# Kernel tuning notes

Hardware: AMD Instinct MI355X
Metric: run time of the kernel (lower is better)

The kernel has to match this reference:

```python
import jax, jax.numpy as jnp
import numpy as np

B, NC, DC = 4, 1024, 256      # batch, codebook entries, codebook dim
K, L = 512, 128               # num_latents, latent_dim
NP, Q = 65536, 64             # query points, queries_dim
LH = 8                        # latent self-attn heads (dim_head 64)
LN_EPS = 1e-5


def _ln(x, g, b):
    m = jnp.mean(x, axis=-1, keepdims=True)
    v = jnp.var(x, axis=-1, keepdims=True)
    return (x - m) * jax.lax.rsqrt(v + LN_EPS) * g + b


def _attn(x, ctx, wq, wkv, wo, bo, h):
    # x: [b,n,dq], ctx: [b,j,dc]; wq: [dq, h*d], wkv: [dc, 2*h*d]
    b, n, _ = x.shape
    j = ctx.shape[1]
    d = wq.shape[1] // h
    q = (x @ wq).reshape(b, n, h, d)
    k, v = jnp.split(ctx @ wkv, 2, axis=-1)
    k = k.reshape(b, j, h, d)
    v = v.reshape(b, j, h, d)
    sim = jnp.einsum('bihd,bjhd->bhij', q, k) * (d ** -0.5)
    a = jax.nn.softmax(sim, axis=-1)
    o = jnp.einsum('bhij,bjhd->bihd', a, v).reshape(b, n, h * d)
    return o @ wo + bo


def _geglu(x):
    a, g = jnp.split(x, 2, axis=-1)
    return a * jax.nn.gelu(g, approximate=False)  # torch F.gelu is exact erf


def setup_inputs() -> dict:
    key = jax.random.key(0)
    ks = iter(jax.random.split(key, 32))
    def w(shape):  # kaiming-ish scaled randn, [in, out] layout
        return jax.random.normal(next(ks), shape, jnp.float32) / np.sqrt(shape[0]).astype(np.float32)
    inp = {
        'codebook': jax.random.normal(next(ks), (B, NC, DC), jnp.float32),
        'queries': jax.random.normal(next(ks), (B, NP, Q), jnp.float32),
        'latents': jax.random.normal(next(ks), (K, L), jnp.float32),
        # CodebookAttention: cross-attn (PreNorm with context norm)
        'ca_ng': jnp.ones((L,)), 'ca_nb': jnp.zeros((L,)),
        'ca_cng': jnp.ones((DC,)), 'ca_cnb': jnp.zeros((DC,)),
        'ca_wq': w((L, 64)), 'ca_wkv': w((DC, 128)), 'ca_wo': w((64, L)), 'ca_bo': jnp.zeros((L,)),
        # cross FF (GEGLU, mult=4)
        'cf_ng': jnp.ones((L,)), 'cf_nb': jnp.zeros((L,)),
        'cf_w1': w((L, 8 * L)), 'cf_b1': jnp.zeros((8 * L,)),
        'cf_w2': w((4 * L, L)), 'cf_b2': jnp.zeros((L,)),
        # latent self-attn (8 heads x 64)
        'sa_ng': jnp.ones((L,)), 'sa_nb': jnp.zeros((L,)),
        'sa_wq': w((L, 512)), 'sa_wkv': w((L, 1024)), 'sa_wo': w((512, L)), 'sa_bo': jnp.zeros((L,)),
        # self FF
        'sf_ng': jnp.ones((L,)), 'sf_nb': jnp.zeros((L,)),
        'sf_w1': w((L, 8 * L)), 'sf_b1': jnp.zeros((8 * L,)),
        'sf_w2': w((4 * L, L)), 'sf_b2': jnp.zeros((L,)),
        # CoordinateAttention: cross-attn
        'qa_ng': jnp.ones((Q,)), 'qa_nb': jnp.zeros((Q,)),
        'qa_cng': jnp.ones((L,)), 'qa_cnb': jnp.zeros((L,)),
        'qa_wq': w((Q, 64)), 'qa_wkv': w((L, 128)), 'qa_wo': w((64, Q)), 'qa_bo': jnp.zeros((Q,)),
        # decoder FF (geglu: hidden = 2*Q, GEGLU halves to Q)
        'qf_ng': jnp.ones((Q,)), 'qf_nb': jnp.zeros((Q,)),
        'qf_w1': w((Q, 2 * Q)), 'qf_b1': jnp.zeros((2 * Q,)),
        'qf_w2': w((Q, Q)), 'qf_b2': jnp.zeros((Q,)),
    }
    return inp


def reference(codebook, queries, latents,
              ca_ng, ca_nb, ca_cng, ca_cnb, ca_wq, ca_wkv, ca_wo, ca_bo,
              cf_ng, cf_nb, cf_w1, cf_b1, cf_w2, cf_b2,
              sa_ng, sa_nb, sa_wq, sa_wkv, sa_wo, sa_bo,
              sf_ng, sf_nb, sf_w1, sf_b1, sf_w2, sf_b2,
              qa_ng, qa_nb, qa_cng, qa_cnb, qa_wq, qa_wkv, qa_wo, qa_bo,
              qf_ng, qf_nb, qf_w1, qf_b1, qf_w2, qf_b2):
    b = codebook.shape[0]
    # ---- CodebookAttention ----
    x = jnp.broadcast_to(latents, (b,) + latents.shape)  # [b,K,L]
    xn = _ln(x, ca_ng, ca_nb)
    cn = _ln(codebook, ca_cng, ca_cnb)
    x = _attn(xn, cn, ca_wq, ca_wkv, ca_wo, ca_bo, 1) + x
    h = _ln(x, cf_ng, cf_nb)
    x = (_geglu(h @ cf_w1 + cf_b1) @ cf_w2 + cf_b2) + x
    xn = _ln(x, sa_ng, sa_nb)
    x = _attn(xn, xn, sa_wq, sa_wkv, sa_wo, sa_bo, LH) + x
    h = _ln(x, sf_ng, sf_nb)
    lat = (_geglu(h @ sf_w1 + sf_b1) @ sf_w2 + sf_b2) + x  # [b,K,L]
    # ---- CoordinateAttention ----
    y = queries  # [b,NP,Q]
    yn = _ln(y, qa_ng, qa_nb)
    cn = _ln(lat, qa_cng, qa_cnb)
    y = _attn(yn, cn, qa_wq, qa_wkv, qa_wo, qa_bo, 1) + y
    h = _ln(y, qf_ng, qf_nb)
    y = (_geglu(h @ qf_w1 + qf_b1) @ qf_w2 + qf_b2) + y
    return y
```

## Files before the change

kernel.cpp:

```cpp
#include <hip/hip_runtime.h>
#include <hip/hip_fp16.h>
#include <math.h>

#define DEV __device__ __forceinline__

typedef _Float16 f16x2 __attribute__((ext_vector_type(2)));

DEV float wsumf(float v){
  #pragma unroll
  for(int m=32;m>=1;m>>=1) v += __shfl_xor(v,m,64);
  return v;
}
DEV float wmaxf(float v){
  #pragma unroll
  for(int m=32;m>=1;m>>=1) v = fmaxf(v,__shfl_xor(v,m,64));
  return v;
}
DEV unsigned pk2(float a, float b){
  f16x2 h; h.x=(_Float16)a; h.y=(_Float16)b;
  return __builtin_bit_cast(unsigned, h);
}
DEV f16x2 u2h(unsigned u){ return __builtin_bit_cast(f16x2, u); }
DEV float fdot2f(f16x2 a, f16x2 b, float c){
#if __has_builtin(__builtin_amdgcn_fdot2)
  return __builtin_amdgcn_fdot2(a,b,c,false);
#else
  return c + (float)a.x*(float)b.x + (float)a.y*(float)b.y;
#endif
}
DEV float gelu_exact(float g){ return 0.5f*g*(1.f+erff(g*0.70710678118654752f)); }


__global__ void k_cb_kv(const float* __restrict__ cb, const float* __restrict__ cng,
                        const float* __restrict__ cnb, const float* __restrict__ wkv,
                        float* __restrict__ kcb, float* __restrict__ vcb){
  int r = blockIdx.x;
  int t = threadIdx.x;
  __shared__ float cn[256]; __shared__ float red[4];
  const float* row = cb + (size_t)r*256;
  float a0 = row[t], a1 = row[t+128];
  float s = wsumf(a0+a1), ss = wsumf(a0*a0+a1*a1);
  int w = t>>6;
  if ((t&63)==0){ red[w] = s; red[2+w] = ss; }
  __syncthreads();
  float mean = (red[0]+red[1])*(1.f/256.f);
  float var  = (red[2]+red[3])*(1.f/256.f) - mean*mean;
  float rstd = rsqrtf(var + 1e-5f);
  cn[t]     = (a0-mean)*rstd*cng[t]+cnb[t];
  cn[t+128] = (a1-mean)*rstd*cng[t+128]+cnb[t+128];
  __syncthreads();
  float acc = 0.f;
  for(int d=0; d<256; d++) acc += cn[d]*wkv[d*128+t];
  if (t<64) kcb[(size_t)r*64 + t] = acc;
  else      vcb[(size_t)r*64 + (t-64)] = acc;
}

__global__ void k_lat_q(const float* __restrict__ latents, const float* __restrict__ ng,
                        const float* __restrict__ nb, const float* __restrict__ wq,
                        float* __restrict__ q1){
  int i = blockIdx.x; int l = threadIdx.x;
  __shared__ float xn[128];
  float a0 = latents[i*128+l], a1 = latents[i*128+64+l];
  float s = wsumf(a0+a1), ss = wsumf(a0*a0+a1*a1);
  float mean = s*(1.f/128.f), var = ss*(1.f/128.f) - mean*mean;
  float rstd = rsqrtf(var+1e-5f);
  xn[l]    = (a0-mean)*rstd*ng[l]+nb[l];
  xn[64+l] = (a1-mean)*rstd*ng[64+l]+nb[64+l];
  __syncthreads();
  float acc=0.f;
  for(int d=0; d<128; d++) acc += xn[d]*wq[d*64+l];
  q1[i*64+l] = acc*0.125f;
}

__global__ void k_attn1(const float* __restrict__ q1, const float* __restrict__ kcb,
                        const float* __restrict__ vcb, const float* __restrict__ wo,
                        const float* __restrict__ bo, const float* __restrict__ latents,
                        float* __restrict__ x1){
  int b = blockIdx.y, i = blockIdx.x, l = threadIdx.x;
  __shared__ float qs[64], as[1024], os[64];
  qs[l] = q1[i*64+l];
  __syncthreads();
  float s[16];
  const float* kb = kcb + (size_t)b*1024*64;
  for(int t=0;t<16;t++){
    int j = l + 64*t; float acc=0.f;
    const float* kr = kb + (size_t)j*64;
    for(int d=0;d<64;d++) acc += qs[d]*kr[d];
    s[t]=acc;
  }
  float m=-1e30f;
  #pragma unroll
  for(int t=0;t<16;t++) m=fmaxf(m,s[t]);
  m=wmaxf(m);
  float sum=0.f;
  #pragma unroll
  for(int t=0;t<16;t++){ s[t]=__expf(s[t]-m); sum+=s[t]; }
  sum = wsumf(sum); float inv = 1.f/sum;
  #pragma unroll
  for(int t=0;t<16;t++) as[l+64*t] = s[t]*inv;
  __syncthreads();
  const float* vb = vcb + (size_t)b*1024*64;
  float o=0.f;
  for(int j=0;j<1024;j++) o += as[j]*vb[(size_t)j*64+l];
  os[l]=o; __syncthreads();
  float r0 = bo[l]    + latents[i*128+l];
  float r1 = bo[64+l] + latents[i*128+64+l];
  for(int d=0;d<64;d++){ float od=os[d]; r0 += od*wo[d*128+l]; r1 += od*wo[d*128+64+l]; }
  size_t ro = ((size_t)b*512+i)*128;
  x1[ro + l] = r0;
  x1[ro + 64+l] = r1;
}

__global__ void k_ffn(const float* __restrict__ xin, const float* __restrict__ ng,
                      const float* __restrict__ nb, const float* __restrict__ w1,
                      const float* __restrict__ b1, const float* __restrict__ w2,
                      const float* __restrict__ b2, float* __restrict__ xout){
  int r = blockIdx.x; int t = threadIdx.x;
  __shared__ float xi[128], h[128], tf[1024], red[8];
  const float* row = xin + (size_t)r*128;
  float a = (t<128)? row[t] : 0.f;
  float s=wsumf(a), ss=wsumf(a*a);
  int w=t>>6;
  if((t&63)==0){red[w]=s; red[4+w]=ss;}
  __syncthreads();
  float mean=(red[0]+red[1]+red[2]+red[3])*(1.f/128.f);
  float var =(red[4]+red[5]+red[6]+red[7])*(1.f/128.f) - mean*mean;
  float rstd=rsqrtf(var+1e-5f);
  if(t<128){ xi[t]=a; h[t]=(a-mean)*rstd*ng[t]+nb[t]; }
  __syncthreads();
  for(int c=t;c<1024;c+=256){
    float acc=b1[c];
    for(int d=0;d<128;d++) acc+=h[d]*w1[d*1024+c];
    tf[c]=acc;
  }
  __syncthreads();
  for(int c=t;c<512;c+=256){
    tf[c] = tf[c]*gelu_exact(tf[512+c]);
  }
  __syncthreads();
  if(t<128){
    float acc=b2[t];
    for(int d=0;d<512;d++) acc+=tf[d]*w2[d*128+t];
    xout[(size_t)r*128+t] = acc + xi[t];
  }
}

__global__ void k_sa_qkv(const float* __restrict__ xin, const float* __restrict__ ng,
                         const float* __restrict__ nb, const float* __restrict__ wq,
                         const float* __restrict__ wkv, float* __restrict__ saq,
                         float* __restrict__ sak, float* __restrict__ sav){
  int r=blockIdx.x, t=threadIdx.x;
  __shared__ float h[128], red[8];
  const float* row = xin + (size_t)r*128;
  float a = (t<128)? row[t]:0.f;
  float s=wsumf(a), ss=wsumf(a*a);
  int w=t>>6;
  if((t&63)==0){red[w]=s; red[4+w]=ss;}
  __syncthreads();
  float mean=(red[0]+red[1]+red[2]+red[3])*(1.f/128.f);
  float var =(red[4]+red[5]+red[6]+red[7])*(1.f/128.f)-mean*mean;
  float rstd=rsqrtf(var+1e-5f);
  if(t<128) h[t]=(a-mean)*rstd*ng[t]+nb[t];
  __syncthreads();
  for(int c=t;c<512;c+=256){
    float aq=0.f, ak=0.f, av=0.f;
    for(int d=0;d<128;d++){
      float hd=h[d];
      aq += hd*wq[d*512+c];
      ak += hd*wkv[d*1024+c];
      av += hd*wkv[d*1024+512+c];
    }
    size_t o=(size_t)r*512+c;
    saq[o]=aq*0.125f; sak[o]=ak; sav[o]=av;
  }
}

__global__ void k_sa_attn(const float* __restrict__ saq, const float* __restrict__ sak,
                          const float* __restrict__ sav, float* __restrict__ sao){
  int b=blockIdx.z, hh=blockIdx.y;
  int w=threadIdx.x>>6, l=threadIdx.x&63;
  int i=blockIdx.x*4+w;
  __shared__ float qs[4][64]; __shared__ float as[4][512];
  qs[w][l]=saq[((size_t)b*512+i)*512+hh*64+l];
  __syncthreads();
  const float* kb = sak + (size_t)b*512*512 + hh*64;
  float s[8];
  #pragma unroll
  for(int t=0;t<8;t++){
    int j=l+64*t; const float* kr=kb+(size_t)j*512; float acc=0.f;
    for(int d=0;d<64;d++) acc+=qs[w][d]*kr[d];
    s[t]=acc;
  }
  float m=-1e30f;
  #pragma unroll
  for(int t=0;t<8;t++) m=fmaxf(m,s[t]);
  m=wmaxf(m);
  float sum=0.f;
  #pragma unroll
  for(int t=0;t<8;t++){ s[t]=__expf(s[t]-m); sum+=s[t]; }
  sum=wsumf(sum);
  float inv=1.f/sum;
  #pragma unroll
  for(int t=0;t<8;t++) as[w][l+64*t]=s[t]*inv;
  __syncthreads();
  const float* vb = sav + (size_t)b*512*512 + hh*64;
  float o=0.f;
  for(int j=0;j<512;j++) o += as[w][j]*vb[(size_t)j*512+l];
  sao[((size_t)b*512+i)*512+hh*64+l]=o;
}

__global__ void k_sa_proj(const float* __restrict__ sao, const float* __restrict__ wo,
                          const float* __restrict__ bo, const float* __restrict__ resid,
                          float* __restrict__ xout){
  int r=blockIdx.x, t=threadIdx.x;
  __shared__ float o[512]; __shared__ float acc2[256];
  o[t]=sao[(size_t)r*512+t]; o[256+t]=sao[(size_t)r*512+256+t];
  __syncthreads();
  int c = t&127; int half = t>>7;
  float acc=0.f;
  int d0 = half*256;
  for(int d=d0; d<d0+256; d++) acc += o[d]*wo[d*128+c];
  acc2[t]=acc; __syncthreads();
  if(t<128) xout[(size_t)r*128+t] = acc2[t]+acc2[t+128]+bo[t]+resid[(size_t)r*128+t];
}

__global__ void k_kv2p(const float* __restrict__ lat, const float* __restrict__ cng,
                       const float* __restrict__ cnb, const float* __restrict__ wkv,
                       unsigned* __restrict__ kp, unsigned* __restrict__ vp){
  int r=blockIdx.x, t=threadIdx.x;
  __shared__ float cn[128]; __shared__ float red[4]; __shared__ float kv[128];
  float a = lat[(size_t)r*128+t];
  float s=wsumf(a), ss=wsumf(a*a);
  int w=t>>6;
  if((t&63)==0){red[w]=s;red[2+w]=ss;}
  __syncthreads();
  float mean=(red[0]+red[1])*(1.f/128.f), var=(red[2]+red[3])*(1.f/128.f)-mean*mean;
  float rstd=rsqrtf(var+1e-5f);
  cn[t]=(a-mean)*rstd*cng[t]+cnb[t];
  __syncthreads();
  float acc=0.f;
  for(int d=0;d<128;d++) acc+=cn[d]*wkv[d*128+t];
  kv[t]=acc;
  __syncthreads();
  if(t<32)               kp[(size_t)r*32 + t]      = pk2(kv[2*t],      kv[2*t+1]);
  else if(t>=64 && t<96) vp[(size_t)r*32 + (t-64)] = pk2(kv[64+2*(t-64)], kv[64+2*(t-64)+1]);
}

#define KLS 0
#define VLS 16384
#define GWQ 32768
#define WOP 34816
#define CSKo 36928
#define CNKo 37440
#define CSF 37952
#define CNF 38016
#define CS2 38080
#define CN2 38112
#define LDSU32 38144

__global__ void __launch_bounds__(512,1) k_coord_pt(
    const float* __restrict__ queries, const unsigned* __restrict__ kp_g,
    const unsigned* __restrict__ vp_g, const float* __restrict__ ng,
    const float* __restrict__ nb, const float* __restrict__ wq,
    const float* __restrict__ wo, const float* __restrict__ bo,
    float* __restrict__ out){
  extern __shared__ unsigned lds[];
  int tid=threadIdx.x;
  int b = blockIdx.x>>7;
  const unsigned* kg=kp_g+(size_t)b*16384;
  const unsigned* vg=vp_g+(size_t)b*16384;
  for(int idx=tid; idx<4096; idx+=512){
    ((uint4*)(lds+KLS))[idx]=((const uint4*)kg)[idx];
    ((uint4*)(lds+VLS))[idx]=((const uint4*)vg)[idx];
  }
  for(int idx=tid; idx<2048; idx+=512){
    int e2=idx>>6, d=idx&63;
    lds[GWQ+idx]=pk2(ng[2*e2]*wq[(2*e2)*64+d], ng[2*e2+1]*wq[(2*e2+1)*64+d]);
  }
  for(int idx=tid; idx<2112; idx+=512){
    int d2=idx>>6, r=idx&63;
    lds[WOP+idx]=(d2<32)? pk2(wo[(2*d2)*64+r], wo[(2*d2+1)*64+r]) : pk2(bo[r],0.f);
  }
  if(tid<64){
    float cs=0.f, cn=0.f;
    for(int e=0;e<64;e++){ float wv=wq[e*64+tid]; cs+=ng[e]*wv; cn+=nb[e]*wv; }
    ((float*)(lds+CSF))[tid]=cs; ((float*)(lds+CNF))[tid]=cn;
  }
  __syncthreads();
  if(tid<32){
    const float* csf=(const float*)(lds+CSF); const float* cnf=(const float*)(lds+CNF);
    lds[CS2+tid]=pk2(csf[2*tid],csf[2*tid+1]);
    lds[CN2+tid]=pk2(cnf[2*tid],cnf[2*tid+1]);
  }
  __syncthreads();
  {
    float a=0.f, c=0.f;
    #pragma unroll 1
    for(int d2=0; d2<32; d2++){
      f16x2 kk=u2h(lds[KLS + tid*32 + d2]);
      a=fdot2f(u2h(lds[CS2+d2]),kk,a);
      c=fdot2f(u2h(lds[CN2+d2]),kk,c);
    }
    ((float*)(lds+CSKo))[tid]=0.125f*a;
    ((float*)(lds+CNKo))[tid]=0.125f*c;
  }
  __syncthreads();

  size_t row=(size_t)blockIdx.x*512 + tid;
  const float* yr=queries+row*64;
  float ysum=0.f, ysq=0.f;
  unsigned yp2[32];
  {
    float4 yv[16];
    #pragma unroll
    for(int i=0;i<16;i++){
      yv[i]=((const float4*)yr)[i];
      ysum += (yv[i].x+yv[i].y)+(yv[i].z+yv[i].w);
      ysq  += yv[i].x*yv[i].x+yv[i].y*yv[i].y+yv[i].z*yv[i].z+yv[i].w*yv[i].w;
    }
    #pragma unroll
    for(int i=0;i<16;i++){
      yp2[2*i]  =pk2(yv[i].x,yv[i].y);
      yp2[2*i+1]=pk2(yv[i].z,yv[i].w);
    }
  }
  float mean=ysum*(1.f/64.f);
  float rstd=rsqrtf(ysq*(1.f/64.f)-mean*mean+1e-5f);
  float rm=rstd*mean;
  float rawq[64];
  #pragma unroll
  for(int d=0;d<64;d++) rawq[d]=0.f;
  #pragma unroll 1
  for(int e2=0;e2<32;e2++){
    const uint4* wr=(const uint4*)(lds+GWQ+e2*64);
    f16x2 ye=u2h(yp2[e2]);
    #pragma unroll
    for(int db=0;db<16;db++){
      uint4 w4=wr[db];
      rawq[4*db+0]=fdot2f(ye,u2h(w4.x),rawq[4*db+0]);
      rawq[4*db+1]=fdot2f(ye,u2h(w4.y),rawq[4*db+1]);
      rawq[4*db+2]=fdot2f(ye,u2h(w4.z),rawq[4*db+2]);
      rawq[4*db+3]=fdot2f(ye,u2h(w4.w),rawq[4*db+3]);
    }
  }
  unsigned rq2[32];
  float sc=0.125f*rstd;
  #pragma unroll
  for(int d2=0;d2<32;d2++) rq2[d2]=pk2(sc*rawq[2*d2],sc*rawq[2*d2+1]);
  const float* cskf=(const float*)(lds+CSKo);
  const float* cnkf=(const float*)(lds+CNKo);
  float m=-1e30f, lsum=0.f;
  f16x2 o2[33];
  #pragma unroll
  for(int d2=0;d2<32;d2++) o2[d2]=u2h(0u);
  #pragma unroll 1
  for(int c=0;c<32;c++){
    float s[16];
    #pragma unroll
    for(int jj=0;jj<16;jj++){
      int j=c*16+jj;
      const uint4* kr=(const uint4*)(lds+KLS+j*32);
      float a0=0.f,a1=0.f,a2=0.f,a3=0.f;
      #pragma unroll
      for(int db=0;db<8;db++){
        uint4 k4=kr[db];
        a0=fdot2f(u2h(rq2[4*db+0]),u2h(k4.x),a0);
        a1=fdot2f(u2h(rq2[4*db+1]),u2h(k4.y),a1);
        a2=fdot2f(u2h(rq2[4*db+2]),u2h(k4.z),a2);
        a3=fdot2f(u2h(rq2[4*db+3]),u2h(k4.w),a3);
      }
      s[jj]=((a0+a1)+(a2+a3)) - rm*cskf[j] + cnkf[j];
    }
    float cm=s[0];
    #pragma unroll
    for(int jj=1;jj<16;jj++) cm=fmaxf(cm,s[jj]);
    float mnew=fmaxf(m,cm);
    float f=__expf(m-mnew);
    m=mnew;
    f16x2 fh; fh.x=fh.y=(_Float16)f;
    #pragma unroll
    for(int d2=0;d2<32;d2++) o2[d2]*=fh;
    lsum*=f;
    #pragma unroll
    for(int jj=0;jj<16;jj++){
      float p=__expf(s[jj]-mnew);
      lsum+=p;
      f16x2 ph; ph.x=ph.y=(_Float16)p;
      const uint4* vr=(const uint4*)(lds+VLS+(c*16+jj)*32);
      #pragma unroll
      for(int db=0;db<8;db++){
        uint4 v4=vr[db];
        o2[4*db+0]+=u2h(v4.x)*ph;
        o2[4*db+1]+=u2h(v4.y)*ph;
        o2[4*db+2]+=u2h(v4.z)*ph;
        o2[4*db+3]+=u2h(v4.w)*ph;
      }
    }
  }
  {
    float invl=1.f/lsum;
    f16x2 ih; ih.x=ih.y=(_Float16)invl;
    #pragma unroll
    for(int d2=0;d2<32;d2++) o2[d2]*=ih;
    o2[32]=u2h(pk2(1.f,0.f));
  }
  float acc[64];
  #pragma unroll
  for(int r=0;r<64;r++) acc[r]=0.f;
  #pragma unroll 1
  for(int d2=0;d2<33;d2++){
    const uint4* wr=(const uint4*)(lds+WOP+d2*64);
    f16x2 od=o2[d2];
    #pragma unroll
    for(int db=0;db<16;db++){
      uint4 w4=wr[db];
      acc[4*db+0]=fdot2f(od,u2h(w4.x),acc[4*db+0]);
      acc[4*db+1]=fdot2f(od,u2h(w4.y),acc[4*db+1]);
      acc[4*db+2]=fdot2f(od,u2h(w4.z),acc[4*db+2]);
      acc[4*db+3]=fdot2f(od,u2h(w4.w),acc[4*db+3]);
    }
  }
  float* orow=out+row*64;
  #pragma unroll
  for(int i=0;i<16;i++){
    float4 yv=((const float4*)yr)[i];
    float4 st;
    st.x=acc[4*i+0]+yv.x; st.y=acc[4*i+1]+yv.y;
    st.z=acc[4*i+2]+yv.z; st.w=acc[4*i+3]+yv.w;
    ((float4*)orow)[i]=st;
  }
}

__global__ void __launch_bounds__(512,1) k_ffq2(
    float* __restrict__ y, const float* __restrict__ ng, const float* __restrict__ nb,
    const float* __restrict__ w1, const float* __restrict__ b1,
    const float* __restrict__ w2, const float* __restrict__ b2){
  __shared__ __align__(16) unsigned gw1p[4096];
  __shared__ __align__(16) unsigned w2p[2112];
  __shared__ float cs1f[128], cn1f[128];
  int tid=threadIdx.x;
  for(int idx=tid;idx<4096;idx+=512){
    int cc=idx>>5, e2=idx&31;
    gw1p[idx]=pk2(ng[2*e2]*w1[(2*e2)*128+cc], ng[2*e2+1]*w1[(2*e2+1)*128+cc]);
  }
  for(int idx=tid;idx<2112;idx+=512){
    int d2=idx>>6, r=idx&63;
    w2p[idx]=(d2<32)? pk2(w2[(2*d2)*64+r], w2[(2*d2+1)*64+r]) : pk2(b2[r],0.f);
  }
  if(tid<128){
    float cs=0.f, cn=0.f;
    for(int e=0;e<64;e++){ float wv=w1[e*128+tid]; cs+=ng[e]*wv; cn+=nb[e]*wv; }
    cs1f[tid]=cs; cn1f[tid]=cn+b1[tid];
  }
  __syncthreads();
  size_t row=(size_t)blockIdx.x*512 + tid;
  float* yrow=y+row*64;
  float ysum=0.f, ysq=0.f;
  unsigned yp2[32];
  {
    float4 yv[16];
    #pragma unroll
    for(int i=0;i<16;i++){
      yv[i]=((const float4*)yrow)[i];
      ysum += (yv[i].x+yv[i].y)+(yv[i].z+yv[i].w);
      ysq  += yv[i].x*yv[i].x+yv[i].y*yv[i].y+yv[i].z*yv[i].z+yv[i].w*yv[i].w;
    }
    float mean=ysum*(1.f/64.f);
    float rstd=rsqrtf(ysq*(1.f/64.f)-mean*mean+1e-5f);
    float rm=rstd*mean;
    #pragma unroll
    for(int i=0;i<16;i++){
      yp2[2*i]  =pk2(rstd*yv[i].x,rstd*yv[i].y);
      yp2[2*i+1]=pk2(rstd*yv[i].z,rstd*yv[i].w);
    }
    ysum=rm;
  }
  float rm=ysum;
  unsigned u2[33];
  #pragma unroll 1
  for(int c=0;c<64;c+=2){
    float uu[2];
    #pragma unroll
    for(int k=0;k<2;k++){
      int cc=c+k;
      const uint4* wa=(const uint4*)&gw1p[cc*32];
      const uint4* wg=(const uint4*)&gw1p[(cc+64)*32];
      float a0=0.f,a1=0.f,g0=0.f,g1=0.f;
      #pragma unroll
      for(int db=0;db<8;db++){
        uint4 A=wa[db], G=wg[db];
        a0=fdot2f(u2h(yp2[4*db+0]),u2h(A.x),a0);
        a1=fdot2f(u2h(yp2[4*db+1]),u2h(A.y),a1);
        a0=fdot2f(u2h(yp2[4*db+2]),u2h(A.z),a0);
        a1=fdot2f(u2h(yp2[4*db+3]),u2h(A.w),a1);
        g0=fdot2f(u2h(yp2[4*db+0]),u2h(G.x),g0);
        g1=fdot2f(u2h(yp2[4*db+1]),u2h(G.y),g1);
        g0=fdot2f(u2h(yp2[4*db+2]),u2h(G.z),g0);
        g1=fdot2f(u2h(yp2[4*db+3]),u2h(G.w),g1);
      }
      float ha=(a0+a1)-rm*cs1f[cc]+cn1f[cc];
      float hg=(g0+g1)-rm*cs1f[cc+64]+cn1f[cc+64];
      uu[k]=ha*gelu_exact(hg);
    }
    u2[c>>1]=pk2(uu[0],uu[1]);
  }
  u2[32]=pk2(1.f,0.f);
  float acc[64];
  #pragma unroll
  for(int r=0;r<64;r++) acc[r]=0.f;
  #pragma unroll 1
  for(int d2=0;d2<33;d2++){
    const uint4* wr=(const uint4*)&w2p[d2*64];
    f16x2 ud=u2h(u2[d2]);
    #pragma unroll
    for(int db=0;db<16;db++){
      uint4 w4=wr[db];
      acc[4*db+0]=fdot2f(ud,u2h(w4.x),acc[4*db+0]);
      acc[4*db+1]=fdot2f(ud,u2h(w4.y),acc[4*db+1]);
      acc[4*db+2]=fdot2f(ud,u2h(w4.z),acc[4*db+2]);
      acc[4*db+3]=fdot2f(ud,u2h(w4.w),acc[4*db+3]);
    }
  }
  #pragma unroll
  for(int i=0;i<16;i++){
    float4 yv=((const float4*)yrow)[i];
    float4 st;
    st.x=acc[4*i+0]+yv.x; st.y=acc[4*i+1]+yv.y;
    st.z=acc[4*i+2]+yv.z; st.w=acc[4*i+3]+yv.w;
    ((float4*)yrow)[i]=st;
  }
}

extern "C" void kernel_launch(void* const* d_in, const int* in_sizes, int n_in,
                              void* d_out, int out_size, void* d_ws, size_t ws_size,
                              hipStream_t stream){
  const float* cb      =(const float*)d_in[0];
  const float* queries =(const float*)d_in[1];
  const float* latents =(const float*)d_in[2];
  const float* ca_ng=(const float*)d_in[3],  *ca_nb=(const float*)d_in[4];
  const float* ca_cng=(const float*)d_in[5], *ca_cnb=(const float*)d_in[6];
  const float* ca_wq=(const float*)d_in[7],  *ca_wkv=(const float*)d_in[8];
  const float* ca_wo=(const float*)d_in[9],  *ca_bo=(const float*)d_in[10];
  const float* cf_ng=(const float*)d_in[11], *cf_nb=(const float*)d_in[12];
  const float* cf_w1=(const float*)d_in[13], *cf_b1=(const float*)d_in[14];
  const float* cf_w2=(const float*)d_in[15], *cf_b2=(const float*)d_in[16];
  const float* sa_ng=(const float*)d_in[17], *sa_nb=(const float*)d_in[18];
  const float* sa_wq=(const float*)d_in[19], *sa_wkv=(const float*)d_in[20];
  const float* sa_wo=(const float*)d_in[21], *sa_bo=(const float*)d_in[22];
  const float* sf_ng=(const float*)d_in[23], *sf_nb=(const float*)d_in[24];
  const float* sf_w1=(const float*)d_in[25], *sf_b1=(const float*)d_in[26];
  const float* sf_w2=(const float*)d_in[27], *sf_b2=(const float*)d_in[28];
  const float* qa_ng=(const float*)d_in[29], *qa_nb=(const float*)d_in[30];
  const float* qa_cng=(const float*)d_in[31],*qa_cnb=(const float*)d_in[32];
  const float* qa_wq=(const float*)d_in[33], *qa_wkv=(const float*)d_in[34];
  const float* qa_wo=(const float*)d_in[35], *qa_bo=(const float*)d_in[36];
  const float* qf_ng=(const float*)d_in[37], *qf_nb=(const float*)d_in[38];
  const float* qf_w1=(const float*)d_in[39], *qf_b1=(const float*)d_in[40];
  const float* qf_w2=(const float*)d_in[41], *qf_b2=(const float*)d_in[42];
  float* out=(float*)d_out;

  float* kcb = out;
  float* vcb = kcb + 262144;
  float* q1  = vcb + 262144;
  float* x1  = q1  + 32768;
  float* x2  = x1  + 262144;
  float* x3  = x2  + 262144;
  float* lat = x3  + 262144;
  float* saq = lat + 262144;
  float* sak = saq + 1048576;
  float* sav = sak + 1048576;
  float* sao = sav + 1048576;

  unsigned* kp=(unsigned*)d_ws;
  unsigned* vp=kp+65536;

  k_cb_kv<<<4096,128,0,stream>>>(cb,ca_cng,ca_cnb,ca_wkv,kcb,vcb);
  k_lat_q<<<512,64,0,stream>>>(latents,ca_ng,ca_nb,ca_wq,q1);
  k_attn1<<<dim3(512,4),64,0,stream>>>(q1,kcb,vcb,ca_wo,ca_bo,latents,x1);
  k_ffn<<<2048,256,0,stream>>>(x1,cf_ng,cf_nb,cf_w1,cf_b1,cf_w2,cf_b2,x2);
  k_sa_qkv<<<2048,256,0,stream>>>(x2,sa_ng,sa_nb,sa_wq,sa_wkv,saq,sak,sav);
  k_sa_attn<<<dim3(128,8,4),256,0,stream>>>(saq,sak,sav,sao);
  k_sa_proj<<<2048,256,0,stream>>>(sao,sa_wo,sa_bo,x2,x3);
  k_ffn<<<2048,256,0,stream>>>(x3,sf_ng,sf_nb,sf_w1,sf_b1,sf_w2,sf_b2,lat);
  k_kv2p<<<2048,128,0,stream>>>(lat,qa_cng,qa_cnb,qa_wkv,kp,vp);
  hipFuncSetAttribute((const void*)k_coord_pt,
                      hipFuncAttributeMaxDynamicSharedMemorySize, LDSU32*4);
  k_coord_pt<<<512,512,LDSU32*4,stream>>>(queries,kp,vp,qa_ng,qa_nb,qa_wq,qa_wo,qa_bo,out);
  k_ffq2<<<512,512,0,stream>>>(out,qf_ng,qf_nb,qf_w1,qf_b1,qf_w2,qf_b2);
}
```

Baseline: 1.811 ms.

## Process two query rows per thread in coord attention and FFN; widen attn1 blocks

The coordinate attention and query FFN kernels now handle two rows per thread, with half as many blocks. Each LDS load of K/V or weights is reused for two rows' dot products, which cuts LDS traffic per row. The cost is roughly double the register pressure from two output accumulator sets, which may cause spills at 512 threads per block. Separately, the first cross-attention kernel goes from 64 to 256 threads per block and reduces softmax and PV partial sums across four waves.

```diff
diff --git a/kernel.cpp b/kernel.cpp
--- a/kernel.cpp
+++ b/kernel.cpp
@@ -76,39 +76,48 @@
                         const float* __restrict__ vcb, const float* __restrict__ wo,
                         const float* __restrict__ bo, const float* __restrict__ latents,
                         float* __restrict__ x1){
-  int b = blockIdx.y, i = blockIdx.x, l = threadIdx.x;
-  __shared__ float qs[64], as[1024], os[64];
-  qs[l] = q1[i*64+l];
-  __syncthreads();
-  float s[16];
-  const float* kb = kcb + (size_t)b*1024*64;
-  for(int t=0;t<16;t++){
-    int j = l + 64*t; float acc=0.f;
+  int b = blockIdx.y, i = blockIdx.x, t = threadIdx.x;
+  int l = t&63, w = t>>6;
+  __shared__ float qs[64], as[1024], red[4][64], redm[4], reds[4], os[64];
+  if(t<64) qs[t] = q1[i*64+t];
+  __syncthreads();
+  const float* kb = kcb + (size_t)b*65536;
+  float s[4];
+  #pragma unroll
+  for(int tt=0;tt<4;tt++){
+    int j = t + 256*tt; float acc=0.f;
     const float* kr = kb + (size_t)j*64;
     for(int d=0;d<64;d++) acc += qs[d]*kr[d];
-    s[t]=acc;
-  }
-  float m=-1e30f;
-  #pragma unroll
-  for(int t=0;t<16;t++) m=fmaxf(m,s[t]);
-  m=wmaxf(m);
+    s[tt]=acc;
+  }
+  float m = fmaxf(fmaxf(s[0],s[1]),fmaxf(s[2],s[3]));
+  m = wmaxf(m);
+  if(l==0) redm[w]=m;
+  __syncthreads();
+  m = fmaxf(fmaxf(redm[0],redm[1]),fmaxf(redm[2],redm[3]));
   float sum=0.f;
   #pragma unroll
-  for(int t=0;t<16;t++){ s[t]=__expf(s[t]-m); sum+=s[t]; }
-  sum = wsumf(sum); float inv = 1.f/sum;
-  #pragma unroll
-  for(int t=0;t<16;t++) as[l+64*t] = s[t]*inv;
-  __syncthreads();
-  const float* vb = vcb + (size_t)b*1024*64;
+  for(int tt=0;tt<4;tt++){ s[tt]=__expf(s[tt]-m); sum+=s[tt]; }
+  sum = wsumf(sum);
+  if(l==0) reds[w]=sum;
+  __syncthreads();
+  sum = reds[0]+reds[1]+reds[2]+reds[3];
+  float inv = 1.f/sum;
+  #pragma unroll
+  for(int tt=0;tt<4;tt++) as[t+256*tt] = s[tt]*inv;
+  __syncthreads();
+  const float* vb = vcb + (size_t)b*65536;
   float o=0.f;
-  for(int j=0;j<1024;j++) o += as[j]*vb[(size_t)j*64+l];
-  os[l]=o; __syncthreads();
-  float r0 = bo[l]    + latents[i*128+l];
-  float r1 = bo[64+l] + latents[i*128+64+l];
-  for(int d=0;d<64;d++){ float od=os[d]; r0 += od*wo[d*128+l]; r1 += od*wo[d*128+64+l]; }
-  size_t ro = ((size_t)b*512+i)*128;
-  x1[ro + l] = r0;
-  x1[ro + 64+l] = r1;
+  for(int j=256*w;j<256*w+256;j++) o += as[j]*vb[(size_t)j*64+l];
+  red[w][l]=o;
+  __syncthreads();
+  if(t<64) os[t]=red[0][t]+red[1][t]+red[2][t]+red[3][t];
+  __syncthreads();
+  if(t<128){
+    float r = bo[t] + latents[i*128+t];
+    for(int d=0;d<64;d++) r += os[d]*wo[d*128+t];
+    x1[((size_t)b*512+i)*128+t] = r;
+  }
 }
 
 __global__ void k_ffn(const float* __restrict__ xin, const float* __restrict__ ng,
@@ -258,6 +267,39 @@
 #define CN2 38112
 #define LDSU32 38144
 
+#define COORD_EPI(OARR, LSUM, ROW) { \
+  float invl=1.f/(LSUM); \
+  f16x2 ih; ih.x=ih.y=(_Float16)invl; \
+  _Pragma("unroll") \
+  for(int d2=0;d2<32;d2++) OARR[d2]*=ih; \
+  OARR[32]=u2h(pk2(1.f,0.f)); \
+  float acc[64]; \
+  _Pragma("unroll") \
+  for(int r=0;r<64;r++) acc[r]=0.f; \
+  _Pragma("unroll 1") \
+  for(int d2=0;d2<33;d2++){ \
+    const uint4* wr=(const uint4*)(lds+WOP+d2*64); \
+    f16x2 od=OARR[d2]; \
+    _Pragma("unroll") \
+    for(int db=0;db<16;db++){ \
+      uint4 w4=wr[db]; \
+      acc[4*db+0]=fdot2f(od,u2h(w4.x),acc[4*db+0]); \
+      acc[4*db+1]=fdot2f(od,u2h(w4.y),acc[4*db+1]); \
+      acc[4*db+2]=fdot2f(od,u2h(w4.z),acc[4*db+2]); \
+      acc[4*db+3]=fdot2f(od,u2h(w4.w),acc[4*db+3]); \
+    } \
+  } \
+  const float* yrr=queries+(ROW)*64; \
+  float* orow=out+(ROW)*64; \
+  _Pragma("unroll") \
+  for(int i=0;i<16;i++){ \
+    float4 yv=((const float4*)yrr)[i]; \
+    float4 st; \
+    st.x=acc[4*i+0]+yv.x; st.y=acc[4*i+1]+yv.y; \
+    st.z=acc[4*i+2]+yv.z; st.w=acc[4*i+3]+yv.w; \
+    ((float4*)orow)[i]=st; \
+  } }
+
 __global__ void __launch_bounds__(512,1) k_coord_pt(
     const float* __restrict__ queries, const unsigned* __restrict__ kp_g,
     const unsigned* __restrict__ vp_g, const float* __restrict__ ng,
@@ -266,7 +308,7 @@
     float* __restrict__ out){
   extern __shared__ unsigned lds[];
   int tid=threadIdx.x;
-  int b = blockIdx.x>>7;
+  int b = blockIdx.x>>6;
   const unsigned* kg=kp_g+(size_t)b*16384;
   const unsigned* vg=vp_g+(size_t)b*16384;
   for(int idx=tid; idx<4096; idx+=512){
@@ -306,130 +348,152 @@
   }
   __syncthreads();
 
-  size_t row=(size_t)blockIdx.x*512 + tid;
-  const float* yr=queries+row*64;
-  float ysum=0.f, ysq=0.f;
-  unsigned yp2[32];
-  {
-    float4 yv[16];
+  size_t row0=(size_t)blockIdx.x*1024 + tid;
+  float rm[2];
+  unsigned rq2[2][32];
+  #pragma unroll
+  for(int p=0;p<2;p++){
+    const float* yr=queries+(row0+(size_t)p*512)*64;
+    float ysum=0.f, ysq=0.f;
+    unsigned yp2[32];
+    {
+      float4 yv[16];
+      #pragma unroll
+      for(int i=0;i<16;i++){
+        yv[i]=((const float4*)yr)[i];
+        ysum += (yv[i].x+yv[i].y)+(yv[i].z+yv[i].w);
+        ysq  += yv[i].x*yv[i].x+yv[i].y*yv[i].y+yv[i].z*yv[i].z+yv[i].w*yv[i].w;
+      }
+      #pragma unroll
+      for(int i=0;i<16;i++){
+        yp2[2*i]  =pk2(yv[i].x,yv[i].y);
+        yp2[2*i+1]=pk2(yv[i].z,yv[i].w);
+      }
+    }
+    float mean=ysum*(1.f/64.f);
+    float rstd=rsqrtf(ysq*(1.f/64.f)-mean*mean+1e-5f);
+    rm[p]=rstd*mean;
+    float rawq[64];
     #pragma unroll
-    for(int i=0;i<16;i++){
-      yv[i]=((const float4*)yr)[i];
-      ysum += (yv[i].x+yv[i].y)+(yv[i].z+yv[i].w);
-      ysq  += yv[i].x*yv[i].x+yv[i].y*yv[i].y+yv[i].z*yv[i].z+yv[i].w*yv[i].w;
-    }
+    for(int d=0;d<64;d++) rawq[d]=0.f;
+    #pragma unroll 1
+    for(int e2=0;e2<32;e2++){
+      const uint4* wr=(const uint4*)(lds+GWQ+e2*64);
+      f16x2 ye=u2h(yp2[e2]);
+      #pragma unroll
+      for(int db=0;db<16;db++){
+        uint4 w4=wr[db];
+        rawq[4*db+0]=fdot2f(ye,u2h(w4.x),rawq[4*db+0]);
+        rawq[4*db+1]=fdot2f(ye,u2h(w4.y),rawq[4*db+1]);
+        rawq[4*db+2]=fdot2f(ye,u2h(w4.z),rawq[4*db+2]);
+        rawq[4*db+3]=fdot2f(ye,u2h(w4.w),rawq[4*db+3]);
+      }
+    }
+    float sc=0.125f*rstd;
     #pragma unroll
-    for(int i=0;i<16;i++){
-      yp2[2*i]  =pk2(yv[i].x,yv[i].y);
-      yp2[2*i+1]=pk2(yv[i].z,yv[i].w);
-    }
-  }
-  float mean=ysum*(1.f/64.f);
-  float rstd=rsqrtf(ysq*(1.f/64.f)-mean*mean+1e-5f);
-  float rm=rstd*mean;
-  float rawq[64];
-  #pragma unroll
-  for(int d=0;d<64;d++) rawq[d]=0.f;
-  #pragma unroll 1
-  for(int e2=0;e2<32;e2++){
-    const uint4* wr=(const uint4*)(lds+GWQ+e2*64);
-    f16x2 ye=u2h(yp2[e2]);
-    #pragma unroll
-    for(int db=0;db<16;db++){
-      uint4 w4=wr[db];
-      rawq[4*db+0]=fdot2f(ye,u2h(w4.x),rawq[4*db+0]);
-      rawq[4*db+1]=fdot2f(ye,u2h(w4.y),rawq[4*db+1]);
-      rawq[4*db+2]=fdot2f(ye,u2h(w4.z),rawq[4*db+2]);
-      rawq[4*db+3]=fdot2f(ye,u2h(w4.w),rawq[4*db+3]);
-    }
-  }
-  unsigned rq2[32];
-  float sc=0.125f*rstd;
-  #pragma unroll
-  for(int d2=0;d2<32;d2++) rq2[d2]=pk2(sc*rawq[2*d2],sc*rawq[2*d2+1]);
+    for(int d2=0;d2<32;d2++) rq2[p][d2]=pk2(sc*rawq[2*d2],sc*rawq[2*d2+1]);
+  }
+
   const float* cskf=(const float*)(lds+CSKo);
   const float* cnkf=(const float*)(lds+CNKo);
-  float m=-1e30f, lsum=0.f;
-  f16x2 o2[33];
-  #pragma unroll
-  for(int d2=0;d2<32;d2++) o2[d2]=u2h(0u);
+  float m0=-1e30f, m1=-1e30f, ls0=0.f, ls1=0.f;
+  f16x2 oA[33], oB[33];
+  #pragma unroll
+  for(int d2=0;d2<32;d2++){ oA[d2]=u2h(0u); oB[d2]=u2h(0u); }
   #pragma unroll 1
-  for(int c=0;c<32;c++){
-    float s[16];
+  for(int c=0;c<64;c++){
+    float s0[8], s1[8];
     #pragma unroll
-    for(int jj=0;jj<16;jj++){
-      int j=c*16+jj;
+    for(int jj=0;jj<8;jj++){
+      int j=c*8+jj;
       const uint4* kr=(const uint4*)(lds+KLS+j*32);
-      float a0=0.f,a1=0.f,a2=0.f,a3=0.f;
+      float a0=0.f,a1=0.f,b0=0.f,b1=0.f;
       #pragma unroll
       for(int db=0;db<8;db++){
         uint4 k4=kr[db];
-        a0=fdot2f(u2h(rq2[4*db+0]),u2h(k4.x),a0);
-        a1=fdot2f(u2h(rq2[4*db+1]),u2h(k4.y),a1);
-        a2=fdot2f(u2h(rq2[4*db+2]),u2h(k4.z),a2);
-        a3=fdot2f(u2h(rq2[4*db+3]),u2h(k4.w),a3);
+        a0=fdot2f(u2h(rq2[0][4*db+0]),u2h(k4.x),a0);
+        a0=fdot2f(u2h(rq2[0][4*db+1]),u2h(k4.y),a0);
+        a1=fdot2f(u2h(rq2[0][4*db+2]),u2h(k4.z),a1);
+        a1=fdot2f(u2h(rq2[0][4*db+3]),u2h(k4.w),a1);
+        b0=fdot2f(u2h(rq2[1][4*db+0]),u2h(k4.x),b0);
+        b0=fdot2f(u2h(rq2[1][4*db+1]),u2h(k4.y),b0);
+        b1=fdot2f(u2h(rq2[1][4*db+2]),u2h(k4.z),b1);
+        b1=fdot2f(u2h(rq2[1][4*db+3]),u2h(k4.w),b1);
       }
-      s[jj]=((a0+a1)+(a2+a3)) - rm*cskf[j] + cnkf[j];
-    }
-    float cm=s[0];
+      s0[jj]=(a0+a1) - rm[0]*cskf[j] + cnkf[j];
+      s1[jj]=(b0+b1) - rm[1]*cskf[j] + cnkf[j];
+    }
+    {
+      float cm=s0[0];
+      #pragma unroll
+      for(int jj=1;jj<8;jj++) cm=fmaxf(cm,s0[jj]);
+      float mn=fmaxf(m0,cm);
+      float f=__expf(m0-mn); m0=mn;
+      f16x2 fh; fh.x=fh.y=(_Float16)f;
+      #pragma unroll
+      for(int d2=0;d2<32;d2++) oA[d2]*=fh;
+      ls0*=f;
+      #pragma unroll
+      for(int jj=0;jj<8;jj++){ s0[jj]=__expf(s0[jj]-mn); ls0+=s0[jj]; }
+    }
+    {
+      float cm=s1[0];
+      #pragma unroll
+      for(int jj=1;jj<8;jj++) cm=fmaxf(cm,s1[jj]);
+      float mn=fmaxf(m1,cm);
+      float f=__expf(m1-mn); m1=mn;
+      f16x2 fh; fh.x=fh.y=(_Float16)f;
+      #pragma unroll
+      for(int d2=0;d2<32;d2++) oB[d2]*=fh;
+      ls1*=f;
+      #pragma unroll
+      for(int jj=0;jj<8;jj++){ s1[jj]=__expf(s1[jj]-mn); ls1+=s1[jj]; }
+    }
     #pragma unroll
-    for(int jj=1;jj<16;jj++) cm=fmaxf(cm,s[jj]);
-    float mnew=fmaxf(m,cm);
-    float f=__expf(m-mnew);
-    m=mnew;
-    f16x2 fh; fh.x=fh.y=(_Float16)f;
-    #pragma unroll
-    for(int d2=0;d2<32;d2++) o2[d2]*=fh;
-    lsum*=f;
-    #pragma unroll
-    for(int jj=0;jj<16;jj++){
-      float p=__expf(s[jj]-mnew);
-      lsum+=p;
-      f16x2 ph; ph.x=ph.y=(_Float16)p;
-      const uint4* vr=(const uint4*)(lds+VLS+(c*16+jj)*32);
+    for(int jj=0;jj<8;jj++){
+      const uint4* vr=(const uint4*)(lds+VLS+(c*8+jj)*32);
+      f16x2 p0; p0.x=p0.y=(_Float16)s0[jj];
+      f16x2 p1; p1.x=p1.y=(_Float16)s1[jj];
       #pragma unroll
       for(int db=0;db<8;db++){
         uint4 v4=vr[db];
-        o2[4*db+0]+=u2h(v4.x)*ph;
-        o2[4*db+1]+=u2h(v4.y)*ph;
-        o2[4*db+2]+=u2h(v4.z)*ph;
-        o2[4*db+3]+=u2h(v4.w)*ph;
+        oA[4*db+0]+=u2h(v4.x)*p0;  oB[4*db+0]+=u2h(v4.x)*p1;
+        oA[4*db+1]+=u2h(v4.y)*p0;  oB[4*db+1]+=u2h(v4.y)*p1;
+        oA[4*db+2]+=u2h(v4.z)*p0;  oB[4*db+2]+=u2h(v4.z)*p1;
+        oA[4*db+3]+=u2h(v4.w)*p0;  oB[4*db+3]+=u2h(v4.w)*p1;
       }
     }
   }
-  {
-    float invl=1.f/lsum;
-    f16x2 ih; ih.x=ih.y=(_Float16)invl;
-    #pragma unroll
-    for(int d2=0;d2<32;d2++) o2[d2]*=ih;
-    o2[32]=u2h(pk2(1.f,0.f));
-  }
-  float acc[64];
-  #pragma unroll
-  for(int r=0;r<64;r++) acc[r]=0.f;
-  #pragma unroll 1
-  for(int d2=0;d2<33;d2++){
-    const uint4* wr=(const uint4*)(lds+WOP+d2*64);
-    f16x2 od=o2[d2];
-    #pragma unroll
-    for(int db=0;db<16;db++){
-      uint4 w4=wr[db];
-      acc[4*db+0]=fdot2f(od,u2h(w4.x),acc[4*db+0]);
-      acc[4*db+1]=fdot2f(od,u2h(w4.y),acc[4*db+1]);
-      acc[4*db+2]=fdot2f(od,u2h(w4.z),acc[4*db+2]);
-      acc[4*db+3]=fdot2f(od,u2h(w4.w),acc[4*db+3]);
-    }
-  }
-  float* orow=out+row*64;
-  #pragma unroll
-  for(int i=0;i<16;i++){
-    float4 yv=((const float4*)yr)[i];
-    float4 st;
-    st.x=acc[4*i+0]+yv.x; st.y=acc[4*i+1]+yv.y;
-    st.z=acc[4*i+2]+yv.z; st.w=acc[4*i+3]+yv.w;
-    ((float4*)orow)[i]=st;
-  }
-}
+  COORD_EPI(oA, ls0, row0)
+  COORD_EPI(oB, ls1, row0+512)
+}
+
+#define FFQ_EPI(UARR, ROW) { \
+  float acc[64]; \
+  _Pragma("unroll") \
+  for(int r=0;r<64;r++) acc[r]=0.f; \
+  _Pragma("unroll 1") \
+  for(int d2=0;d2<33;d2++){ \
+    const uint4* wr=(const uint4*)&w2p[d2*64]; \
+    f16x2 ud=u2h(UARR[d2]); \
+    _Pragma("unroll") \
+    for(int db=0;db<16;db++){ \
+      uint4 w4=wr[db]; \
+      acc[4*db+0]=fdot2f(ud,u2h(w4.x),acc[4*db+0]); \
+      acc[4*db+1]=fdot2f(ud,u2h(w4.y),acc[4*db+1]); \
+      acc[4*db+2]=fdot2f(ud,u2h(w4.z),acc[4*db+2]); \
+      acc[4*db+3]=fdot2f(ud,u2h(w4.w),acc[4*db+3]); \
+    } \
+  } \
+  float* yrw=y+(ROW)*64; \
+  _Pragma("unroll") \
+  for(int i=0;i<16;i++){ \
+    float4 yv=((const float4*)yrw)[i]; \
+    float4 st; \
+    st.x=acc[4*i+0]+yv.x; st.y=acc[4*i+1]+yv.y; \
+    st.z=acc[4*i+2]+yv.z; st.w=acc[4*i+3]+yv.w; \
+    ((float4*)yrw)[i]=st; \
+  } }
 
 __global__ void __launch_bounds__(512,1) k_ffq2(
     float* __restrict__ y, const float* __restrict__ ng, const float* __restrict__ nb,
@@ -453,11 +517,13 @@
     cs1f[tid]=cs; cn1f[tid]=cn+b1[tid];
   }
   __syncthreads();
-  size_t row=(size_t)blockIdx.x*512 + tid;
-  float* yrow=y+row*64;
-  float ysum=0.f, ysq=0.f;
-  unsigned yp2[32];
-  {
+  size_t row0=(size_t)blockIdx.x*1024 + tid;
+  unsigned yp2[2][32];
+  float rm[2];
+  #pragma unroll
+  for(int p=0;p<2;p++){
+    const float* yrow=y+(row0+(size_t)p*512)*64;
+    float ysum=0.f, ysq=0.f;
     float4 yv[16];
     #pragma unroll
     for(int i=0;i<16;i++){
@@ -467,68 +533,57 @@
     }
     float mean=ysum*(1.f/64.f);
     float rstd=rsqrtf(ysq*(1.f/64.f)-mean*mean+1e-5f);
-    float rm=rstd*mean;
+    rm[p]=rstd*mean;
     #pragma unroll
     for(int i=0;i<16;i++){
-      yp2[2*i]  =pk2(rstd*yv[i].x,rstd*yv[i].y);
-      yp2[2*i+1]=pk2(rstd*yv[i].z,rstd*yv[i].w);
-    }
-    ysum=rm;
-  }
-  float rm=ysum;
-  unsigned u2[33];
+      yp2[p][2*i]  =pk2(rstd*yv[i].x,rstd*yv[i].y);
+      yp2[p][2*i+1]=pk2(rstd*yv[i].z,rstd*yv[i].w);
+    }
+  }
+  unsigned uA[33], uB[33];
   #pragma unroll 1
   for(int c=0;c<64;c+=2){
-    float uu[2];
+    float u0[2], u1[2];
     #pragma unroll
     for(int k=0;k<2;k++){
       int cc=c+k;
       const uint4* wa=(const uint4*)&gw1p[cc*32];
       const uint4* wg=(const uint4*)&gw1p[(cc+64)*32];
-      float a0=0.f,a1=0.f,g0=0.f,g1=0.f;
+      float a0=0.f,g0=0.f,a1=0.f,g1=0.f;
       #pragma unroll
       for(int db=0;db<8;db++){
         uint4 A=wa[db], G=wg[db];
-        a0=fdot2f(u2h(yp2[4*db+0]),u2h(A.x),a0);
-        a1=fdot2f(u2h(yp2[4*db+1]),u2h(A.y),a1);
-        a0=fdot2f(u2h(yp2[4*db+2]),u2h(A.z),a0);
-        a1=fdot2f(u2h(yp2[4*db+3]),u2h(A.w),a1);
-        g0=fdot2f(u2h(yp2[4*db+0]),u2h(G.x),g0);
-        g1=fdot2f(u2h(yp2[4*db+1]),u2h(G.y),g1);
-        g0=fdot2f(u2h(yp2[4*db+2]),u2h(G.z),g0);
-        g1=fdot2f(u2h(yp2[4*db+3]),u2h(G.w),g1);
+        a0=fdot2f(u2h(yp2[0][4*db+0]),u2h(A.x),a0);
+        a0=fdot2f(u2h(yp2[0][4*db+1]),u2h(A.y),a0);
+        a0=fdot2f(u2h(yp2[0][4*db+2]),u2h(A.z),a0);
+        a0=fdot2f(u2h(yp2[0][4*db+3]),u2h(A.w),a0);
+        g0=fdot2f(u2h(yp2[0][4*db+0]),u2h(G.x),g0);
+        g0=fdot2f(u2h(yp2[0][4*db+1]),u2h(G.y),g0);
+        g0=fdot2f(u2h(yp2[0][4*db+2]),u2h(G.z),g0);
+        g0=fdot2f(u2h(yp2[0][4*db+3]),u2h(G.w),g0);
+        a1=fdot2f(u2h(yp2[1][4*db+0]),u2h(A.x),a1);
+        a1=fdot2f(u2h(yp2[1][4*db+1]),u2h(A.y),a1);
+        a1=fdot2f(u2h(yp2[1][4*db+2]),u2h(A.z),a1);
+        a1=fdot2f(u2h(yp2[1][4*db+3]),u2h(A.w),a1);
+        g1=fdot2f(u2h(yp2[1][4*db+0]),u2h(G.x),g1);
+        g1=fdot2f(u2h(yp2[1][4*db+1]),u2h(G.y),g1);
+        g1=fdot2f(u2h(yp2[1][4*db+2]),u2h(G.z),g1);
+        g1=fdot2f(u2h(yp2[1][4*db+3]),u2h(G.w),g1);
       }
-      float ha=(a0+a1)-rm*cs1f[cc]+cn1f[cc];
-      float hg=(g0+g1)-rm*cs1f[cc+64]+cn1f[cc+64];
-      uu[k]=ha*gelu_exact(hg);
-    }
-    u2[c>>1]=pk2(uu[0],uu[1]);
-  }
-  u2[32]=pk2(1.f,0.f);
-  float acc[64];
-  #pragma unroll
-  for(int r=0;r<64;r++) acc[r]=0.f;
-  #pragma unroll 1
-  for(int d2=0;d2<33;d2++){
-    const uint4* wr=(const uint4*)&w2p[d2*64];
-    f16x2 ud=u2h(u2[d2]);
-    #pragma unroll
-    for(int db=0;db<16;db++){
-      uint4 w4=wr[db];
-      acc[4*db+0]=fdot2f(ud,u2h(w4.x),acc[4*db+0]);
-      acc[4*db+1]=fdot2f(ud,u2h(w4.y),acc[4*db+1]);
-      acc[4*db+2]=fdot2f(ud,u2h(w4.z),acc[4*db+2]);
-      acc[4*db+3]=fdot2f(ud,u2h(w4.w),acc[4*db+3]);
-    }
-  }
-  #pragma unroll
-  for(int i=0;i<16;i++){
-    float4 yv=((const float4*)yrow)[i];
-    float4 st;
-    st.x=acc[4*i+0]+yv.x; st.y=acc[4*i+1]+yv.y;
-    st.z=acc[4*i+2]+yv.z; st.w=acc[4*i+3]+yv.w;
-    ((float4*)yrow)[i]=st;
-  }
+      float ha0=a0-rm[0]*cs1f[cc]+cn1f[cc];
+      float hg0=g0-rm[0]*cs1f[cc+64]+cn1f[cc+64];
+      float ha1=a1-rm[1]*cs1f[cc]+cn1f[cc];
+      float hg1=g1-rm[1]*cs1f[cc+64]+cn1f[cc+64];
+      u0[k]=ha0*gelu_exact(hg0);
+      u1[k]=ha1*gelu_exact(hg1);
+    }
+    uA[c>>1]=pk2(u0[0],u0[1]);
+    uB[c>>1]=pk2(u1[0],u1[1]);
+  }
+  uA[32]=pk2(1.f,0.f);
+  uB[32]=pk2(1.f,0.f);
+  FFQ_EPI(uA, row0)
+  FFQ_EPI(uB, row0+512)
 }
 
 extern "C" void kernel_launch(void* const* d_in, const int* in_sizes, int n_in,
@@ -576,7 +631,7 @@
 
   k_cb_kv<<<4096,128,0,stream>>>(cb,ca_cng,ca_cnb,ca_wkv,kcb,vcb);
   k_lat_q<<<512,64,0,stream>>>(latents,ca_ng,ca_nb,ca_wq,q1);
-  k_attn1<<<dim3(512,4),64,0,stream>>>(q1,kcb,vcb,ca_wo,ca_bo,latents,x1);
+  k_attn1<<<dim3(512,4),256,0,stream>>>(q1,kcb,vcb,ca_wo,ca_bo,latents,x1);
   k_ffn<<<2048,256,0,stream>>>(x1,cf_ng,cf_nb,cf_w1,cf_b1,cf_w2,cf_b2,x2);
   k_sa_qkv<<<2048,256,0,stream>>>(x2,sa_ng,sa_nb,sa_wq,sa_wkv,saq,sak,sav);
   k_sa_attn<<<dim3(128,8,4),256,0,stream>>>(saq,sak,sav,sao);
@@ -585,6 +640,6 @@
   k_kv2p<<<2048,128,0,stream>>>(lat,qa_cng,qa_cnb,qa_wkv,kp,vp);
   hipFuncSetAttribute((const void*)k_coord_pt,
                       hipFuncAttributeMaxDynamicSharedMemorySize, LDSU32*4);
-  k_coord_pt<<<512,512,LDSU32*4,stream>>>(queries,kp,vp,qa_ng,qa_nb,qa_wq,qa_wo,qa_bo,out);
-  k_ffq2<<<512,512,0,stream>>>(out,qf_ng,qf_nb,qf_w1,qf_b1,qf_w2,qf_b2);
-}
+  k_coord_pt<<<256,512,LDSU32*4,stream>>>(queries,kp,vp,qa_ng,qa_nb,qa_wq,qa_wo,qa_bo,out);
+  k_ffq2<<<256,512,0,stream>>>(out,qf_ng,qf_nb,qf_w1,qf_b1,qf_w2,qf_b2);
+}
```

Measured after the change: 1.685 ms. 7.0% less time.
